# Kernel tuning notes

Measured on AMD Instinct MI355X. Metric: run time of the kernel, lower is better.

The kernel has to match this reference:

```python
import jax, jax.numpy as jnp
import numpy as np

# FreqEncoder constants (from init_kwargs)
X_DIM = 3
MIN_DEG = 0.0
MAX_DEG = 8.0
NUM_SCALES = 8            # max_deg - min_deg
RES = 128                 # 2 ** log2_res
NUM_CH = 8                # num_feats (channels per grid)
STD = 0.001
P = 262144                # number of sample points


def setup_inputs() -> dict:
    key = jax.random.key(0)
    k1, k2 = jax.random.split(key)
    x = jax.random.uniform(k1, (P, X_DIM), dtype=jnp.float32)
    # learned 1D grids: [num_scales*2*x_dim, num_channels, res]
    features = jax.random.normal(k2, (NUM_SCALES * 2 * X_DIM, NUM_CH, RES), dtype=jnp.float32) * STD
    return {"x": x, "features": features}


def reference(x, features):
    S, D, C, res = NUM_SCALES, X_DIM, NUM_CH, RES
    N = S * 2 * D  # number of 1D grids
    p = x.shape[0]

    # scales = 2 ** linspace(min_deg, max_deg, num_scales)  (matches torch.linspace)
    scales = 2.0 ** jnp.linspace(MIN_DEG, MAX_DEG, S).astype(x.dtype)  # [S]

    xb = x[:, None, :] * scales[None, :, None]                     # [P, S, D]
    latent = jnp.sin(jnp.stack([xb, xb + 0.5 * jnp.pi], axis=-2))  # [P, S, 2, D]

    # values in [-1, 1] used as grid_sample y-coords; one grid per (s, phase, d)
    v = latent.reshape(p, N).T                                     # [N, P]

    # align_corners=True bilinear unnormalization along the res axis
    pos = (v + 1.0) * 0.5 * (res - 1)                              # [N, P] in [0, res-1]
    i0f = jnp.floor(pos)
    frac = pos - i0f                                               # [N, P]
    i0 = jnp.clip(i0f, 0, res - 1).astype(jnp.int32)
    i1 = jnp.clip(i0 + 1, 0, res - 1)

    idx0 = jnp.broadcast_to(i0[:, None, :], (N, C, p))
    idx1 = jnp.broadcast_to(i1[:, None, :], (N, C, p))
    f0 = jnp.take_along_axis(features, idx0, axis=2)               # [N, C, P]
    f1 = jnp.take_along_axis(features, idx1, axis=2)               # [N, C, P]
    fs = f0 * (1.0 - frac[:, None, :]) + f1 * frac[:, None, :]     # [N, C, P]

    # [N, C, P] -> [S, 2, D, C, P] -> [P, C, S, 2, D], add residual, flatten
    fs = fs.reshape(S, 2, D, C, p).transpose(4, 3, 0, 1, 2)
    out = (fs + latent[:, None, :, :, :]).reshape(p, C * S * 2 * D)

    # use_identity=True: prepend raw coordinates
    return jnp.concatenate([x, out], axis=-1)                      # [P, 3 + 384]
```

## Files before the change

kernel.cpp:

```cpp
#include <hip/hip_runtime.h>
#include <hip/hip_bf16.h>
#include <stdint.h>


constexpr int P_PTS = 262144;
constexpr int S_SC  = 8;
constexpr int D_DIM = 3;
constexpr int C_CH  = 8;
constexpr int RES   = 128;
constexpr int N_GR  = S_SC * 2 * D_DIM;
constexpr int OW    = 3 + C_CH * N_GR;
constexpr int KPB   = 16;
constexpr int CHUNKS = 16;
constexpr int PPB   = KPB * CHUNKS;
constexpr int BLK   = 1024;

constexpr float ENC_SCALE = 256.0f;
constexpr float DEC_SCALE = 1.0f / 256.0f;
constexpr float INV_2PI   = 0.15915494309189535f;

constexpr int LDS_TABLE_B = N_GR * RES * 8;
constexpr int LDS_SOUT_B  = KPB * OW * 4;
constexpr int LDS_SX_B    = PPB * D_DIM * 4;
constexpr int LDS_TOTAL_B = LDS_TABLE_B + LDS_SOUT_B + LDS_SX_B;

typedef float f32x2 __attribute__((ext_vector_type(2)));
typedef float f32x4 __attribute__((ext_vector_type(4)));

__device__ uint2 g_tap[N_GR * RES];

__global__ __launch_bounds__(256) void feat_pack_kernel(const float* __restrict__ f) {
    int t = blockIdx.x * 256 + threadIdx.x;
    if (t >= N_GR * RES) return;
    int n = t / RES, i = t % RES;

    uint32_t d0, d1;
    {
        float a = f[(n * C_CH + 0) * RES + i] * ENC_SCALE;
        float b = f[(n * C_CH + 1) * RES + i] * ENC_SCALE;
        float c = f[(n * C_CH + 2) * RES + i] * ENC_SCALE;
        float e = f[(n * C_CH + 3) * RES + i] * ENC_SCALE;
        int lo = __builtin_amdgcn_cvt_pk_fp8_f32(a, b, 0, false);
        d0 = (uint32_t)__builtin_amdgcn_cvt_pk_fp8_f32(c, e, lo, true);
    }
    {
        float a = f[(n * C_CH + 4) * RES + i] * ENC_SCALE;
        float b = f[(n * C_CH + 5) * RES + i] * ENC_SCALE;
        float c = f[(n * C_CH + 6) * RES + i] * ENC_SCALE;
        float e = f[(n * C_CH + 7) * RES + i] * ENC_SCALE;
        int lo = __builtin_amdgcn_cvt_pk_fp8_f32(a, b, 0, false);
        d1 = (uint32_t)__builtin_amdgcn_cvt_pk_fp8_f32(c, e, lo, true);
    }
    g_tap[t] = make_uint2(d0, d1);
}

__global__ __launch_bounds__(1024, 8) void freq_encode_kernel(const float* __restrict__ x,
                                                              float* __restrict__ out) {
    extern __shared__ char smem[];
    uint2* ld_tap = reinterpret_cast<uint2*>(smem);
    float* s_out  = reinterpret_cast<float*>(smem + LDS_TABLE_B);
    float* s_x    = reinterpret_cast<float*>(smem + LDS_TABLE_B + LDS_SOUT_B);

    const int tid   = threadIdx.x;
    const int pbase = blockIdx.x * PPB;

    for (int i = tid; i < N_GR * RES; i += BLK) ld_tap[i] = g_tap[i];
    if (tid < PPB * D_DIM) s_x[tid] = x[(size_t)pbase * D_DIM + tid];
    __syncthreads();

    for (int ch = 0; ch < CHUNKS; ++ch) {
        const int p0l = ch * KPB;

        if (tid < KPB * D_DIM) {
            s_out[(tid / D_DIM) * OW + (tid % D_DIM)] = s_x[p0l * D_DIM + tid];
        }

        if (tid < KPB * N_GR) {
            int pl = tid / N_GR;
            int n  = tid % N_GR;
            int s  = n / (2 * D_DIM);
            int r  = n % (2 * D_DIM);
            int ph = r / D_DIM;
            int d  = r % D_DIM;

            float xv    = s_x[(p0l + pl) * D_DIM + d];
            float scale = exp2f((float)s * (8.0f / 7.0f));
            float rv    = fmaf(xv * scale, INV_2PI, ph ? 0.25f : 0.0f);
            float lat   = __builtin_amdgcn_sinf(__builtin_amdgcn_fractf(rv));

            float pos  = (lat + 1.0f) * 63.5f;
            float i0f  = floorf(pos);
            float frac = pos - i0f;
            int   i0   = (int)i0f;
            i0 = max(0, min(i0, RES - 1));
            int   i1   = min(i0 + 1, RES - 1);

            uint2 t0 = ld_tap[n * RES + i0];
            uint2 t1 = ld_tap[n * RES + i1];

            f32x2 a01 = __builtin_amdgcn_cvt_pk_f32_fp8(t0.x, false);
            f32x2 a23 = __builtin_amdgcn_cvt_pk_f32_fp8(t0.x, true);
            f32x2 a45 = __builtin_amdgcn_cvt_pk_f32_fp8(t0.y, false);
            f32x2 a67 = __builtin_amdgcn_cvt_pk_f32_fp8(t0.y, true);
            f32x2 b01 = __builtin_amdgcn_cvt_pk_f32_fp8(t1.x, false);
            f32x2 b23 = __builtin_amdgcn_cvt_pk_f32_fp8(t1.x, true);
            f32x2 b45 = __builtin_amdgcn_cvt_pk_f32_fp8(t1.y, false);
            f32x2 b67 = __builtin_amdgcn_cvt_pk_f32_fp8(t1.y, true);

            float omd = (1.0f - frac) * DEC_SCALE;
            float frd = frac * DEC_SCALE;

            float* dst = &s_out[pl * OW + 3 + n];
            dst[0 * N_GR] = fmaf(a01[0], omd, fmaf(b01[0], frd, lat));
            dst[1 * N_GR] = fmaf(a01[1], omd, fmaf(b01[1], frd, lat));
            dst[2 * N_GR] = fmaf(a23[0], omd, fmaf(b23[0], frd, lat));
            dst[3 * N_GR] = fmaf(a23[1], omd, fmaf(b23[1], frd, lat));
            dst[4 * N_GR] = fmaf(a45[0], omd, fmaf(b45[0], frd, lat));
            dst[5 * N_GR] = fmaf(a45[1], omd, fmaf(b45[1], frd, lat));
            dst[6 * N_GR] = fmaf(a67[0], omd, fmaf(b67[0], frd, lat));
            dst[7 * N_GR] = fmaf(a67[1], omd, fmaf(b67[1], frd, lat));
        }
        __syncthreads();

        constexpr int NV = KPB * OW / 4;
        const f32x4* src = reinterpret_cast<const f32x4*>(s_out);
        f32x4*       dst = reinterpret_cast<f32x4*>(out + ((size_t)pbase + p0l) * OW);
        for (int i = tid; i < NV; i += BLK) {
            __builtin_nontemporal_store(src[i], &dst[i]);
        }
        __syncthreads();
    }
}

extern "C" void kernel_launch(void* const* d_in, const int* in_sizes, int n_in,
                              void* d_out, int out_size, void* d_ws, size_t ws_size,
                              hipStream_t stream) {
    const float* x    = (const float*)d_in[0];
    const float* feat = (const float*)d_in[1];
    float*       out  = (float*)d_out;

    int n_taps = N_GR * RES;
    feat_pack_kernel<<<(n_taps + 255) / 256, 256, 0, stream>>>(feat);

    freq_encode_kernel<<<P_PTS / PPB, BLK, LDS_TOTAL_B, stream>>>(x, out);
}
```

Measured before the change: 101.4 us.

## Write encoder outputs directly to global memory, dropping LDS staging and barriers

Removes the per-chunk shared-memory output staging and the two barriers per chunk. Every thread now handles 16 (point, grid) tasks spread over all 1024 threads and stores its 8 channel values straight to global memory with strided scalar stores. x is read directly from global memory instead of from a staged copy. This gets rid of the idle threads (only 768 of 1024 were active before) and the synchronisation cost. In exchange, the nontemporal 16-byte coalesced stores become scattered 4-byte stores at a stride of 48 floats, which may hurt write efficiency on this write-bound kernel.

```diff
diff --git a/kernel.cpp b/kernel.cpp
--- a/kernel.cpp
+++ b/kernel.cpp
@@ -10,22 +10,16 @@
 constexpr int RES   = 128;
 constexpr int N_GR  = S_SC * 2 * D_DIM;
 constexpr int OW    = 3 + C_CH * N_GR;
-constexpr int KPB   = 16;
-constexpr int CHUNKS = 16;
-constexpr int PPB   = KPB * CHUNKS;
 constexpr int BLK   = 1024;
+constexpr int T_PER = 16;
+constexpr int N_TASKS = P_PTS * N_GR;
+constexpr int N_BLOCKS = N_TASKS / (BLK * T_PER);
 
 constexpr float ENC_SCALE = 256.0f;
 constexpr float DEC_SCALE = 1.0f / 256.0f;
 constexpr float INV_2PI   = 0.15915494309189535f;
 
-constexpr int LDS_TABLE_B = N_GR * RES * 8;
-constexpr int LDS_SOUT_B  = KPB * OW * 4;
-constexpr int LDS_SX_B    = PPB * D_DIM * 4;
-constexpr int LDS_TOTAL_B = LDS_TABLE_B + LDS_SOUT_B + LDS_SX_B;
-
 typedef float f32x2 __attribute__((ext_vector_type(2)));
-typedef float f32x4 __attribute__((ext_vector_type(4)));
 
 __device__ uint2 g_tap[N_GR * RES];
 
@@ -54,81 +48,64 @@
     g_tap[t] = make_uint2(d0, d1);
 }
 
-__global__ __launch_bounds__(1024, 8) void freq_encode_kernel(const float* __restrict__ x,
+__global__ __launch_bounds__(1024, 4) void freq_encode_kernel(const float* __restrict__ x,
                                                               float* __restrict__ out) {
-    extern __shared__ char smem[];
-    uint2* ld_tap = reinterpret_cast<uint2*>(smem);
-    float* s_out  = reinterpret_cast<float*>(smem + LDS_TABLE_B);
-    float* s_x    = reinterpret_cast<float*>(smem + LDS_TABLE_B + LDS_SOUT_B);
+    __shared__ uint2 s_tap[N_GR * RES];
 
-    const int tid   = threadIdx.x;
-    const int pbase = blockIdx.x * PPB;
-
-    for (int i = tid; i < N_GR * RES; i += BLK) ld_tap[i] = g_tap[i];
-    if (tid < PPB * D_DIM) s_x[tid] = x[(size_t)pbase * D_DIM + tid];
+    const int tid = threadIdx.x;
+    for (int i = tid; i < N_GR * RES; i += BLK) s_tap[i] = g_tap[i];
     __syncthreads();
 
-    for (int ch = 0; ch < CHUNKS; ++ch) {
-        const int p0l = ch * KPB;
+    const int base = blockIdx.x * (BLK * T_PER);
 
-        if (tid < KPB * D_DIM) {
-            s_out[(tid / D_DIM) * OW + (tid % D_DIM)] = s_x[p0l * D_DIM + tid];
-        }
+    for (int k = 0; k < T_PER; ++k) {
+        int t  = base + k * BLK + tid;
+        int p  = t / N_GR;
+        int n  = t % N_GR;
+        int s  = n / (2 * D_DIM);
+        int r  = n % (2 * D_DIM);
+        int ph = r / D_DIM;
+        int d  = r % D_DIM;
 
-        if (tid < KPB * N_GR) {
-            int pl = tid / N_GR;
-            int n  = tid % N_GR;
-            int s  = n / (2 * D_DIM);
-            int r  = n % (2 * D_DIM);
-            int ph = r / D_DIM;
-            int d  = r % D_DIM;
+        float xv    = x[p * D_DIM + d];
+        float scale = exp2f((float)s * (8.0f / 7.0f));
+        float rv    = fmaf(xv * scale, INV_2PI, ph ? 0.25f : 0.0f);
+        float lat   = __builtin_amdgcn_sinf(__builtin_amdgcn_fractf(rv));
 
-            float xv    = s_x[(p0l + pl) * D_DIM + d];
-            float scale = exp2f((float)s * (8.0f / 7.0f));
-            float rv    = fmaf(xv * scale, INV_2PI, ph ? 0.25f : 0.0f);
-            float lat   = __builtin_amdgcn_sinf(__builtin_amdgcn_fractf(rv));
+        float pos  = (lat + 1.0f) * 63.5f;
+        float i0f  = floorf(pos);
+        float frac = pos - i0f;
+        int   i0   = (int)i0f;
+        i0 = max(0, min(i0, RES - 1));
+        int   i1   = min(i0 + 1, RES - 1);
 
-            float pos  = (lat + 1.0f) * 63.5f;
-            float i0f  = floorf(pos);
-            float frac = pos - i0f;
-            int   i0   = (int)i0f;
-            i0 = max(0, min(i0, RES - 1));
-            int   i1   = min(i0 + 1, RES - 1);
+        uint2 t0 = s_tap[n * RES + i0];
+        uint2 t1 = s_tap[n * RES + i1];
 
-            uint2 t0 = ld_tap[n * RES + i0];
-            uint2 t1 = ld_tap[n * RES + i1];
+        f32x2 a01 = __builtin_amdgcn_cvt_pk_f32_fp8(t0.x, false);
+        f32x2 a23 = __builtin_amdgcn_cvt_pk_f32_fp8(t0.x, true);
+        f32x2 a45 = __builtin_amdgcn_cvt_pk_f32_fp8(t0.y, false);
+        f32x2 a67 = __builtin_amdgcn_cvt_pk_f32_fp8(t0.y, true);
+        f32x2 b01 = __builtin_amdgcn_cvt_pk_f32_fp8(t1.x, false);
+        f32x2 b23 = __builtin_amdgcn_cvt_pk_f32_fp8(t1.x, true);
+        f32x2 b45 = __builtin_amdgcn_cvt_pk_f32_fp8(t1.y, false);
+        f32x2 b67 = __builtin_amdgcn_cvt_pk_f32_fp8(t1.y, true);
 
-            f32x2 a01 = __builtin_amdgcn_cvt_pk_f32_fp8(t0.x, false);
-            f32x2 a23 = __builtin_amdgcn_cvt_pk_f32_fp8(t0.x, true);
-            f32x2 a45 = __builtin_amdgcn_cvt_pk_f32_fp8(t0.y, false);
-            f32x2 a67 = __builtin_amdgcn_cvt_pk_f32_fp8(t0.y, true);
-            f32x2 b01 = __builtin_amdgcn_cvt_pk_f32_fp8(t1.x, false);
-            f32x2 b23 = __builtin_amdgcn_cvt_pk_f32_fp8(t1.x, true);
-            f32x2 b45 = __builtin_amdgcn_cvt_pk_f32_fp8(t1.y, false);
-            f32x2 b67 = __builtin_amdgcn_cvt_pk_f32_fp8(t1.y, true);
+        float omd = (1.0f - frac) * DEC_SCALE;
+        float frd = frac * DEC_SCALE;
 
-            float omd = (1.0f - frac) * DEC_SCALE;
-            float frd = frac * DEC_SCALE;
+        float* row = out + (size_t)p * OW;
+        if (n < D_DIM) row[n] = xv;
 
-            float* dst = &s_out[pl * OW + 3 + n];
-            dst[0 * N_GR] = fmaf(a01[0], omd, fmaf(b01[0], frd, lat));
-            dst[1 * N_GR] = fmaf(a01[1], omd, fmaf(b01[1], frd, lat));
-            dst[2 * N_GR] = fmaf(a23[0], omd, fmaf(b23[0], frd, lat));
-            dst[3 * N_GR] = fmaf(a23[1], omd, fmaf(b23[1], frd, lat));
-            dst[4 * N_GR] = fmaf(a45[0], omd, fmaf(b45[0], frd, lat));
-            dst[5 * N_GR] = fmaf(a45[1], omd, fmaf(b45[1], frd, lat));
-            dst[6 * N_GR] = fmaf(a67[0], omd, fmaf(b67[0], frd, lat));
-            dst[7 * N_GR] = fmaf(a67[1], omd, fmaf(b67[1], frd, lat));
-        }
-        __syncthreads();
-
-        constexpr int NV = KPB * OW / 4;
-        const f32x4* src = reinterpret_cast<const f32x4*>(s_out);
-        f32x4*       dst = reinterpret_cast<f32x4*>(out + ((size_t)pbase + p0l) * OW);
-        for (int i = tid; i < NV; i += BLK) {
-            __builtin_nontemporal_store(src[i], &dst[i]);
-        }
-        __syncthreads();
+        float* dst = row + 3 + n;
+        dst[0 * N_GR] = fmaf(a01[0], omd, fmaf(b01[0], frd, lat));
+        dst[1 * N_GR] = fmaf(a01[1], omd, fmaf(b01[1], frd, lat));
+        dst[2 * N_GR] = fmaf(a23[0], omd, fmaf(b23[0], frd, lat));
+        dst[3 * N_GR] = fmaf(a23[1], omd, fmaf(b23[1], frd, lat));
+        dst[4 * N_GR] = fmaf(a45[0], omd, fmaf(b45[0], frd, lat));
+        dst[5 * N_GR] = fmaf(a45[1], omd, fmaf(b45[1], frd, lat));
+        dst[6 * N_GR] = fmaf(a67[0], omd, fmaf(b67[0], frd, lat));
+        dst[7 * N_GR] = fmaf(a67[1], omd, fmaf(b67[1], frd, lat));
     }
 }
 
@@ -142,5 +119,5 @@
     int n_taps = N_GR * RES;
     feat_pack_kernel<<<(n_taps + 255) / 256, 256, 0, stream>>>(feat);
 
-    freq_encode_kernel<<<P_PTS / PPB, BLK, LDS_TOTAL_B, stream>>>(x, out);
+    freq_encode_kernel<<<N_BLOCKS, BLK, 0, stream>>>(x, out);
 }
```

Measured after the change: 139.6 us. +37.7%, slower.
